# Performance work log

Hardware: AMD Instinct MI355X
Metric: run time of the kernel (lower is better)

## Reference

```python
import jax, jax.numpy as jnp
import numpy as np


def setup_inputs() -> dict:
    key = jax.random.key(0)
    k1, k2 = jax.random.split(key)
    B, C, H, W = 4, 256, 64, 64
    hw = 1024  # hs = ws = 32, rate = H/hs = 2
    ori_x = jax.random.normal(k1, (B, C, H, W), dtype=jnp.float32)
    scores = jax.random.uniform(k2, (B, hw, hw), dtype=jnp.float32)
    alpha = jnp.ones((1,), dtype=jnp.float32)
    return {"ori_x": ori_x, "scores": scores, "alpha": alpha}


def reference(ori_x, scores, alpha):
    # GroupConvAttention forward for H=W=64 (no bilinear resize branch taken,
    # matching the torch code's else-branch), rate even (no extra rep-pad).
    B, C, H, W = ori_x.shape
    hw = scores.shape[2]
    hs = int(np.sqrt(hw)); ws = hs
    rate = H // hs               # 2
    vk = 2 * rate                # vksize = 4
    pad = rate // 2              # vpadding = 1 (rate even)

    # extract_patches: ReplicationPad2d(pad) + unfold(kernel=vk, stride=rate)
    x_pad = jnp.pad(ori_x, ((0, 0), (0, 0), (pad, pad), (pad, pad)), mode="edge")
    # gather index grids: patch (m,n), intra-patch (u,v)
    ri = (jnp.arange(hs) * rate)[:, None] + jnp.arange(vk)[None, :]  # [hs, vk]
    ci = (jnp.arange(ws) * rate)[:, None] + jnp.arange(vk)[None, :]  # [ws, vk]
    R = ri[:, None, :, None]   # [hs,1,vk,1]
    Cc = ci[None, :, None, :]  # [1,ws,1,vk]
    value = x_pad[:, :, R, Cc]  # [B, C, hs, ws, vk, vk]

    # conv_transpose2d(scores_, value, stride=rate, padding=pad, groups=B)
    # == per query grid cell (Q,R): combined patch = sum_p scores[b,q,p]*value[b,p]
    s = scores.reshape(B, hs, ws, hs, ws)  # [b, Qy, Qx, my, mx]
    P = jnp.einsum("bQRmn,bcmnuv->bcQRuv", s, value)  # [B,C,hs,ws,vk,vk]

    # overlap-add patches at stride `rate` into padded canvas, then crop padding
    canvas = jnp.zeros((B, C, (hs - 1) * rate + vk, (ws - 1) * rate + vk), P.dtype)
    canvas = canvas.at[:, :, R, Cc].add(P)
    y = canvas[:, :, pad:pad + H, pad:pad + W] / 4.0

    return ori_x + y * alpha
```

## Files before the change

kernel.cpp:

```cpp
#include <hip/hip_runtime.h>
#include <hip/hip_bf16.h>
#include <hip/hip_fp16.h>

#define BB 4
#define CC 256
#define HH 64
#define WW 64
#define QRN 1024
#define KN  1024
#define NN  4096
#define KDIM 1120
#define MROWS 1024
#define TROWS 1089

typedef _Float16 f16x8 __attribute__((ext_vector_type(8)));
typedef float f32x4 __attribute__((ext_vector_type(4)));
typedef float f32x16 __attribute__((ext_vector_type(16)));

#define TP_ELEMS ((size_t)BB * TROWS * KDIM)
#define BP_ELEMS ((size_t)16 * CC * KDIM)


#define T_BLOCKS 1089
#define PER_B    1249
#define TB_NWG   (BB * PER_B)

__global__ __launch_bounds__(256)
void build_TB(const float* __restrict__ s, const float* __restrict__ x,
              _Float16* __restrict__ T, _Float16* __restrict__ Bp) {
    const int orig = blockIdx.x;
    const int xcd = orig & 7, pos = orig >> 3;
    const int q = TB_NWG / 8, r = TB_NWG % 8;
    const int wgid =
        (xcd < r ? xcd * (q + 1) : r * (q + 1) + (xcd - r) * q) + pos;

    const int b = wgid / PER_B;
    const int rem = wgid - b * PER_B;
    const int t = threadIdx.x;

    if (rem < T_BLOCKS) {
        const int qr = rem;
        const int Qa = (qr * 993) >> 15;
        const int Ra = qr - 33 * Qa;
        const bool q0 = (Qa < 32), q1 = (Qa >= 1);
        const bool r0 = (Ra < 32), r1 = (Ra >= 1);
        const float* sb = s + (size_t)b * QRN * KN;
        const float* rb00 = sb + ((size_t)((Qa)     * 32 + (Ra)))     * KN;
        const float* rb01 = sb + ((size_t)((Qa)     * 32 + (Ra - 1))) * KN;
        const float* rb10 = sb + ((size_t)((Qa - 1) * 32 + (Ra)))     * KN;
        const float* rb11 = sb + ((size_t)((Qa - 1) * 32 + (Ra - 1))) * KN;
        _Float16* trow = T + ((size_t)b * TROWS + qr) * KDIM;

        float v[5];
        #pragma unroll
        for (int j = 0; j < 5; ++j) {
            const int k = j * 256 + t;
            v[j] = 0.f;
            if (k < KDIM) {
                const int mp = (k * 993) >> 15;
                const int np = k - 33 * mp;
                const bool m0 = (mp < 32), m1 = (mp >= 1) && (mp < 33);
                const bool n0 = (np < 32), n1 = (np >= 1);
                const int col = (mp << 5) + np;
                if (q0 & r0 & m0 & n0) v[j] += rb00[col];
                if (q0 & r1 & m0 & n1) v[j] += rb01[col - 1];
                if (q1 & r0 & m1 & n0) v[j] += rb10[col - 32];
                if (q1 & r1 & m1 & n1) v[j] += rb11[col - 33];
            }
        }
        #pragma unroll
        for (int j = 0; j < 5; ++j) {
            const int k = j * 256 + t;
            if (k < KDIM) trow[k] = (_Float16)v[j];
        }
    } else {
        const int u = rem - T_BLOCKS;
        const int rest = u / 5;
        const int kc = u - rest * 5;
        const int cls = rest >> 3, cg = rest & 7;
        const int k = kc * 256 + t;
        if (k >= KDIM) return;
        const int ph = cls >> 1, pw = cls & 1;
        const int ua = 1 - ph, va = 1 - pw;
        const int bc = b * 4 + cls;

        const int mp = (k * 993) >> 15;
        const int np = k - 33 * mp;
        int rr = 2 * mp + ua - 1; rr = min(max(rr, 0), HH - 1);
        int cc2 = 2 * np + va - 1; cc2 = min(max(cc2, 0), WW - 1);
        const int off = rr * WW + cc2;

        const float* xb = x + ((size_t)b * CC + cg * 32) * HH * WW;
        _Float16* bpb = Bp + ((size_t)bc * CC + cg * 32) * KDIM + k;

        #pragma unroll 8
        for (int i = 0; i < 32; ++i) {
            bpb[(size_t)i * KDIM] = (_Float16)xb[(size_t)i * HH * WW + off];
        }
    }
}

#define A_SLOT 520
#define B_SLOT 1040
#define PF 4
#define NT 35
__global__ __launch_bounds__(256)
void gemm_f16(const _Float16* __restrict__ T,
              const _Float16* __restrict__ Bp,
              const float* __restrict__ orix,
              const float* __restrict__ alphap,
              float* __restrict__ out) {
    __shared__ __align__(16) char smem[32768];
    _Float16* AmB = (_Float16*)smem;
    _Float16* BnB = AmB + 2 * 4 * A_SLOT;
    float*    ex  = (float*)smem;

    const int lin = blockIdx.x + 4 * (blockIdx.y + 8 * blockIdx.z);
    const int wid = (lin & 7) * 64 + (lin >> 3);
    const int bc  = wid >> 5;
    const int byy = (wid >> 2) & 7;
    const int bxx = wid & 3;

    const int b = bc >> 2, cls = bc & 3;
    const int ph = cls >> 1, pw = cls & 1;
    const int c0  = bxx * 64;
    const int px0 = byy * 128;

    const int t = threadIdx.x;
    const int wv = t >> 6, l = t & 63;
    const int lr = l & 31;
    const int lh = l >> 5;
    const int wc = wv & 1;
    const int ks = wv >> 1;

    const _Float16* Ag = Bp + ((size_t)bc * CC + c0) * KDIM;
    const _Float16* Tg = T + (size_t)b * TROWS * KDIM;

    const int st_row  = t >> 2;
    const int st_slot = t & 3;
    const int pxa = px0 + st_row, pxb = px0 + st_row + 64;
    const int trow0 = ((pxa >> 5) + ph) * 33 + (pxa & 31) + pw;
    const int trow1 = ((pxb >> 5) + ph) * 33 + (pxb & 31) + pw;

    f32x16 acc[2][2];
    #pragma unroll
    for (int i = 0; i < 2; ++i)
        #pragma unroll
        for (int j = 0; j < 2; ++j)
            acc[i][j] = (f32x16)(0.f);

    f16x8 rga[PF], rgb0[PF], rgb1[PF];

    #pragma unroll
    for (int s2 = 0; s2 < PF; ++s2) {
        const size_t kb = s2 * 32 + st_slot * 8;
        rga[s2]  = *reinterpret_cast<const f16x8*>(Ag + (size_t)st_row * KDIM + kb);
        rgb0[s2] = *reinterpret_cast<const f16x8*>(Tg + (size_t)trow0 * KDIM + kb);
        rgb1[s2] = *reinterpret_cast<const f16x8*>(Tg + (size_t)trow1 * KDIM + kb);
    }
    *reinterpret_cast<f16x8*>(&AmB[st_slot * A_SLOT + st_row * 8]) = rga[0];
    *reinterpret_cast<f16x8*>(&BnB[st_slot * B_SLOT + st_row * 8]) = rgb0[0];
    *reinterpret_cast<f16x8*>(&BnB[st_slot * B_SLOT + (st_row + 64) * 8]) = rgb1[0];
    asm volatile("s_waitcnt lgkmcnt(0)" ::: "memory");
    __builtin_amdgcn_s_barrier();

    #pragma unroll
    for (int ts = 0; ts < NT; ++ts) {
        const int cur = ts & 1;
        if (ts + PF < NT) {
            const int sl = ts & 3;
            const size_t kb = (size_t)(ts + PF) * 32 + st_slot * 8;
            rga[sl]  = *reinterpret_cast<const f16x8*>(Ag + (size_t)st_row * KDIM + kb);
            rgb0[sl] = *reinterpret_cast<const f16x8*>(Tg + (size_t)trow0 * KDIM + kb);
            rgb1[sl] = *reinterpret_cast<const f16x8*>(Tg + (size_t)trow1 * KDIM + kb);
        }

        const int slot = ks * 2 + lh;
        f16x8 af[2], bf[2];
        #pragma unroll
        for (int mt = 0; mt < 2; ++mt)
            af[mt] = *reinterpret_cast<const f16x8*>(
                &AmB[cur * 4 * A_SLOT + slot * A_SLOT + (mt * 32 + lr) * 8]);
        #pragma unroll
        for (int nt2 = 0; nt2 < 2; ++nt2)
            bf[nt2] = *reinterpret_cast<const f16x8*>(
                &BnB[cur * 4 * B_SLOT + slot * B_SLOT +
                     (wc * 64 + nt2 * 32 + lr) * 8]);
        __builtin_amdgcn_s_setprio(1);
        #pragma unroll
        for (int mt = 0; mt < 2; ++mt)
            #pragma unroll
            for (int nt2 = 0; nt2 < 2; ++nt2)
                acc[mt][nt2] = __builtin_amdgcn_mfma_f32_32x32x16_f16(
                    af[mt], bf[nt2], acc[mt][nt2], 0, 0, 0);
        __builtin_amdgcn_s_setprio(0);

        if (ts + 1 < NT) {
            const int ns = (ts + 1) & 3, nb = cur ^ 1;
            *reinterpret_cast<f16x8*>(&AmB[nb * 4 * A_SLOT + st_slot * A_SLOT + st_row * 8]) = rga[ns];
            *reinterpret_cast<f16x8*>(&BnB[nb * 4 * B_SLOT + st_slot * B_SLOT + st_row * 8]) = rgb0[ns];
            *reinterpret_cast<f16x8*>(&BnB[nb * 4 * B_SLOT + st_slot * B_SLOT + (st_row + 64) * 8]) = rgb1[ns];
        }
        asm volatile("s_waitcnt lgkmcnt(0)" ::: "memory");
        __builtin_amdgcn_s_barrier();
    }

    if (ks == 1) {
        #pragma unroll
        for (int mt = 0; mt < 2; ++mt)
            #pragma unroll
            for (int nt2 = 0; nt2 < 2; ++nt2)
                #pragma unroll
                for (int r = 0; r < 16; ++r)
                    ex[((((mt * 2 + nt2) * 2 + wc) * 16) + r) * 64 + l] =
                        acc[mt][nt2][r];
    }
    asm volatile("s_waitcnt lgkmcnt(0)" ::: "memory");
    __builtin_amdgcn_s_barrier();

    if (ks == 0) {
        const float scale = 0.25f * alphap[0];
        #pragma unroll
        for (int mt = 0; mt < 2; ++mt) {
            #pragma unroll
            for (int nt2 = 0; nt2 < 2; ++nt2) {
                #pragma unroll
                for (int r = 0; r < 16; ++r) {
                    float vsum = acc[mt][nt2][r] +
                        ex[((((mt * 2 + nt2) * 2 + wc) * 16) + r) * 64 + l];
                    int c  = c0 + mt * 32 + (r & 3) + 8 * (r >> 2) + 4 * lh;
                    int px = px0 + wc * 64 + nt2 * 32 + lr;
                    int hh = px >> 5, ww2 = px & 31;
                    int h = 2 * hh + ph, wp = 2 * ww2 + pw;
                    size_t idx = (((size_t)b * CC + c) * HH + h) * WW + wp;
                    out[idx] = orix[idx] + scale * vsum;
                }
            }
        }
    }
}

#define TILE_M 64
#define TILE_N 64
#define TILE_K 16

__global__ void copy_kernel(const float* __restrict__ src,
                            float* __restrict__ dst, int n4) {
    int i = blockIdx.x * blockDim.x + threadIdx.x;
    if (i < n4)
        reinterpret_cast<float4*>(dst)[i] =
            reinterpret_cast<const float4*>(src)[i];
}

__global__ void transpose_kernel(const float* __restrict__ x,
                                 float* __restrict__ xT) {
    __shared__ float tile[32][33];
    int bh = blockIdx.z;
    int b = bh >> 6, h = bh & 63;
    int c0 = blockIdx.y * 32, w0 = blockIdx.x * 32;
    int tw = threadIdx.x & 31;
    int tc = threadIdx.x >> 5;
    #pragma unroll
    for (int i = 0; i < 4; ++i) {
        int c = tc + i * 8;
        tile[c][tw] = x[(((size_t)b * CC + c0 + c) * HH + h) * WW + w0 + tw];
    }
    __syncthreads();
    int tcw = threadIdx.x & 31;
    int twr = threadIdx.x >> 5;
    #pragma unroll
    for (int i = 0; i < 4; ++i) {
        int w = twr + i * 8;
        xT[(((size_t)b * HH + h) * WW + w0 + w) * CC + c0 + tcw] = tile[tcw][w];
    }
}

__global__ __launch_bounds__(256)
void pgemm_scatter(const float* __restrict__ scores,
                   const float* __restrict__ xT,
                   const float* __restrict__ x,
                   const float* __restrict__ alpha,
                   float* __restrict__ out,
                   int use_xt) {
    __shared__ float As[TILE_K][TILE_M];
    __shared__ float Bs[TILE_K][TILE_N];

    const int b      = blockIdx.z;
    const int tile_n = blockIdx.x;
    const int m0     = blockIdx.y * TILE_M;
    const int uv     = tile_n >> 2;
    const int u      = uv >> 2, v = uv & 3;
    const int c0     = (tile_n & 3) * 64;

    const int t  = threadIdx.x;
    const int tx = t & 15;
    const int ty = t >> 4;

    float acc[4][4] = {};
    const float* sb = scores + (size_t)b * QRN * KN;

    for (int k0 = 0; k0 < KN; k0 += TILE_K) {
        {
            int mr = t >> 2;
            int kc = (t & 3) * 4;
            float4 av = *reinterpret_cast<const float4*>(
                sb + (size_t)(m0 + mr) * KN + k0 + kc);
            As[kc + 0][mr] = av.x;
            As[kc + 1][mr] = av.y;
            As[kc + 2][mr] = av.z;
            As[kc + 3][mr] = av.w;
        }
        {
            int kr = t >> 4;
            int kg = k0 + kr;
            int m  = kg >> 5, n = kg & 31;
            int rr = 2 * m + u - 1; rr = min(max(rr, 0), HH - 1);
            int cc = 2 * n + v - 1; cc = min(max(cc, 0), WW - 1);
            int ccol = (t & 15) * 4;
            if (use_xt) {
                float4 bv = *reinterpret_cast<const float4*>(
                    xT + ((((size_t)b * HH + rr) * WW + cc) * CC) + c0 + ccol);
                Bs[kr][ccol + 0] = bv.x;
                Bs[kr][ccol + 1] = bv.y;
                Bs[kr][ccol + 2] = bv.z;
                Bs[kr][ccol + 3] = bv.w;
            } else {
                #pragma unroll
                for (int j = 0; j < 4; ++j) {
                    int c = c0 + ccol + j;
                    Bs[kr][ccol + j] =
                        x[(((size_t)b * CC + c) * HH + rr) * WW + cc];
                }
            }
        }
        __syncthreads();

        #pragma unroll
        for (int k = 0; k < TILE_K; ++k) {
            float a4[4], b4[4];
            *reinterpret_cast<float4*>(a4) =
                *reinterpret_cast<const float4*>(&As[k][ty * 4]);
            *reinterpret_cast<float4*>(b4) =
                *reinterpret_cast<const float4*>(&Bs[k][tx * 4]);
            #pragma unroll
            for (int i = 0; i < 4; ++i)
                #pragma unroll
                for (int j = 0; j < 4; ++j)
                    acc[i][j] += a4[i] * b4[j];
        }
        __syncthreads();
    }

    const float scale = alpha[0] * 0.25f;
    #pragma unroll
    for (int i = 0; i < 4; ++i) {
        int qr = m0 + ty * 4 + i;
        int Q = qr >> 5, R = qr & 31;
        int h = 2 * Q + u - 1;
        int w = 2 * R + v - 1;
        if (h < 0 || h >= HH || w < 0 || w >= WW) continue;
        #pragma unroll
        for (int j = 0; j < 4; ++j) {
            int c = c0 + tx * 4 + j;
            atomicAdd(&out[(((size_t)b * CC + c) * HH + h) * WW + w],
                      acc[i][j] * scale);
        }
    }
}

extern "C" void kernel_launch(void* const* d_in, const int* in_sizes, int n_in,
                              void* d_out, int out_size, void* d_ws,
                              size_t ws_size, hipStream_t stream) {
    const float* ori_x  = (const float*)d_in[0];
    const float* scores = (const float*)d_in[1];
    const float* alpha  = (const float*)d_in[2];
    float* out = (float*)d_out;

    const size_t need_fast = (TP_ELEMS + BP_ELEMS) * sizeof(_Float16);

    if (ws_size >= need_fast) {
        _Float16* T  = (_Float16*)d_ws;
        _Float16* Bp = T + TP_ELEMS;

        build_TB<<<dim3(TB_NWG), 256, 0, stream>>>(scores, ori_x, T, Bp);
        gemm_f16<<<dim3(4, 8, 16), 256, 0, stream>>>(T, Bp, ori_x, alpha, out);
    } else {
        float* xT = (float*)d_ws;
        const size_t xt_bytes = (size_t)BB * HH * WW * CC * sizeof(float);
        const int use_xt = (ws_size >= xt_bytes) ? 1 : 0;

        copy_kernel<<<(BB * CC * HH * WW / 4 + 255) / 256, 256, 0, stream>>>(
            ori_x, out, BB * CC * HH * WW / 4);
        if (use_xt)
            transpose_kernel<<<dim3(WW / 32, CC / 32, BB * HH), 256, 0,
                               stream>>>(ori_x, xT);
        pgemm_scatter<<<dim3(NN / TILE_N, QRN / TILE_M, BB), 256, 0, stream>>>(
            scores, xT, ori_x, alpha, out, use_xt);
    }
}
```

Measured before the change: 48.98 us.

## Double GEMM K-step per barrier and build two T rows per block

The f16 GEMM now consumes 64 K-elements per pipeline step instead of 32. Each thread stages more rows and slots, the register prefetch depth drops from 4 to 2, and LDS grows to about 49 KB. This roughly halves the number of barrier/LDS-store rounds and pads KDIM to 1152 so the steps divide evenly. The build kernel also handles two T rows per workgroup to cut launch overhead, at the cost of some extra padded work and higher register and LDS pressure.

```diff
diff --git a/kernel.cpp b/kernel.cpp
--- a/kernel.cpp
+++ b/kernel.cpp
@@ -8,9 +8,7 @@
 #define WW 64
 #define QRN 1024
 #define KN  1024
-#define NN  4096
-#define KDIM 1120
-#define MROWS 1024
+#define KDIM 1152
 #define TROWS 1089
 
 typedef _Float16 f16x8 __attribute__((ext_vector_type(8)));
@@ -21,8 +19,45 @@
 #define BP_ELEMS ((size_t)16 * CC * KDIM)
 
 
-#define T_BLOCKS 1089
-#define PER_B    1249
+__device__ __forceinline__
+void process_qr(const float* __restrict__ sb, _Float16* __restrict__ T,
+                int b, int qr, int t) {
+    const int Qa = (qr * 993) >> 15;
+    const int Ra = qr - 33 * Qa;
+    const bool q0 = (Qa < 32), q1 = (Qa >= 1);
+    const bool r0 = (Ra < 32), r1 = (Ra >= 1);
+    const float* rb00 = sb + ((size_t)((Qa)     * 32 + (Ra)))     * KN;
+    const float* rb01 = sb + ((size_t)((Qa)     * 32 + (Ra - 1))) * KN;
+    const float* rb10 = sb + ((size_t)((Qa - 1) * 32 + (Ra)))     * KN;
+    const float* rb11 = sb + ((size_t)((Qa - 1) * 32 + (Ra - 1))) * KN;
+    _Float16* trow = T + ((size_t)b * TROWS + qr) * KDIM;
+
+    float v[5];
+    #pragma unroll
+    for (int j = 0; j < 5; ++j) {
+        const int k = j * 256 + t;
+        v[j] = 0.f;
+        if (k < KDIM) {
+            const int mp = (k * 993) >> 15;
+            const int np = k - 33 * mp;
+            const bool m0 = (mp < 32), m1 = (mp >= 1) && (mp < 33);
+            const bool n0 = (np < 32), n1 = (np >= 1);
+            const int col = (mp << 5) + np;
+            if (q0 & r0 & m0 & n0) v[j] += rb00[col];
+            if (q0 & r1 & m0 & n1) v[j] += rb01[col - 1];
+            if (q1 & r0 & m1 & n0) v[j] += rb10[col - 32];
+            if (q1 & r1 & m1 & n1) v[j] += rb11[col - 33];
+        }
+    }
+    #pragma unroll
+    for (int j = 0; j < 5; ++j) {
+        const int k = j * 256 + t;
+        if (k < KDIM) trow[k] = (_Float16)v[j];
+    }
+}
+
+#define T_BLOCKS 545
+#define PER_B    705
 #define TB_NWG   (BB * PER_B)
 
 __global__ __launch_bounds__(256)
@@ -39,40 +74,10 @@
     const int t = threadIdx.x;
 
     if (rem < T_BLOCKS) {
-        const int qr = rem;
-        const int Qa = (qr * 993) >> 15;
-        const int Ra = qr - 33 * Qa;
-        const bool q0 = (Qa < 32), q1 = (Qa >= 1);
-        const bool r0 = (Ra < 32), r1 = (Ra >= 1);
         const float* sb = s + (size_t)b * QRN * KN;
-        const float* rb00 = sb + ((size_t)((Qa)     * 32 + (Ra)))     * KN;
-        const float* rb01 = sb + ((size_t)((Qa)     * 32 + (Ra - 1))) * KN;
-        const float* rb10 = sb + ((size_t)((Qa - 1) * 32 + (Ra)))     * KN;
-        const float* rb11 = sb + ((size_t)((Qa - 1) * 32 + (Ra - 1))) * KN;
-        _Float16* trow = T + ((size_t)b * TROWS + qr) * KDIM;
-
-        float v[5];
-        #pragma unroll
-        for (int j = 0; j < 5; ++j) {
-            const int k = j * 256 + t;
-            v[j] = 0.f;
-            if (k < KDIM) {
-                const int mp = (k * 993) >> 15;
-                const int np = k - 33 * mp;
-                const bool m0 = (mp < 32), m1 = (mp >= 1) && (mp < 33);
-                const bool n0 = (np < 32), n1 = (np >= 1);
-                const int col = (mp << 5) + np;
-                if (q0 & r0 & m0 & n0) v[j] += rb00[col];
-                if (q0 & r1 & m0 & n1) v[j] += rb01[col - 1];
-                if (q1 & r0 & m1 & n0) v[j] += rb10[col - 32];
-                if (q1 & r1 & m1 & n1) v[j] += rb11[col - 33];
-            }
-        }
-        #pragma unroll
-        for (int j = 0; j < 5; ++j) {
-            const int k = j * 256 + t;
-            if (k < KDIM) trow[k] = (_Float16)v[j];
-        }
+        const int qr0 = rem * 2;
+        process_qr(sb, T, b, qr0, t);
+        if (qr0 + 1 < TROWS) process_qr(sb, T, b, qr0 + 1, t);
     } else {
         const int u = rem - T_BLOCKS;
         const int rest = u / 5;
@@ -102,17 +107,18 @@
 
 #define A_SLOT 520
 #define B_SLOT 1040
-#define PF 4
-#define NT 35
+#define A_BUF  (8 * A_SLOT)
+#define B_BUF  (8 * B_SLOT)
+#define NSTEP  18
 __global__ __launch_bounds__(256)
 void gemm_f16(const _Float16* __restrict__ T,
               const _Float16* __restrict__ Bp,
               const float* __restrict__ orix,
               const float* __restrict__ alphap,
               float* __restrict__ out) {
-    __shared__ __align__(16) char smem[32768];
+    __shared__ __align__(16) char smem[49920];
     _Float16* AmB = (_Float16*)smem;
-    _Float16* BnB = AmB + 2 * 4 * A_SLOT;
+    _Float16* BnB = AmB + 2 * A_BUF;
     float*    ex  = (float*)smem;
 
     const int lin = blockIdx.x + 4 * (blockIdx.y + 8 * blockIdx.z);
@@ -136,11 +142,15 @@
     const _Float16* Ag = Bp + ((size_t)bc * CC + c0) * KDIM;
     const _Float16* Tg = T + (size_t)b * TROWS * KDIM;
 
-    const int st_row  = t >> 2;
-    const int st_slot = t & 3;
-    const int pxa = px0 + st_row, pxb = px0 + st_row + 64;
-    const int trow0 = ((pxa >> 5) + ph) * 33 + (pxa & 31) + pw;
-    const int trow1 = ((pxb >> 5) + ph) * 33 + (pxb & 31) + pw;
+    const int st_r    = t >> 3;
+    const int st_slot = t & 7;
+    const int kb0     = st_slot * 8;
+    int trowv[4];
+    #pragma unroll
+    for (int r2 = 0; r2 < 4; ++r2) {
+        const int px = px0 + r2 * 32 + st_r;
+        trowv[r2] = ((px >> 5) + ph) * 33 + (px & 31) + pw;
+    }
 
     f32x16 acc[2][2];
     #pragma unroll
@@ -149,57 +159,77 @@
         for (int j = 0; j < 2; ++j)
             acc[i][j] = (f32x16)(0.f);
 
-    f16x8 rga[PF], rgb0[PF], rgb1[PF];
-
-    #pragma unroll
-    for (int s2 = 0; s2 < PF; ++s2) {
-        const size_t kb = s2 * 32 + st_slot * 8;
-        rga[s2]  = *reinterpret_cast<const f16x8*>(Ag + (size_t)st_row * KDIM + kb);
-        rgb0[s2] = *reinterpret_cast<const f16x8*>(Tg + (size_t)trow0 * KDIM + kb);
-        rgb1[s2] = *reinterpret_cast<const f16x8*>(Tg + (size_t)trow1 * KDIM + kb);
-    }
-    *reinterpret_cast<f16x8*>(&AmB[st_slot * A_SLOT + st_row * 8]) = rga[0];
-    *reinterpret_cast<f16x8*>(&BnB[st_slot * B_SLOT + st_row * 8]) = rgb0[0];
-    *reinterpret_cast<f16x8*>(&BnB[st_slot * B_SLOT + (st_row + 64) * 8]) = rgb1[0];
+    f16x8 rga[2][2], rgb[2][4];
+
+    #pragma unroll
+    for (int s2 = 0; s2 < 2; ++s2) {
+        const size_t kb = (size_t)s2 * 64 + kb0;
+        rga[s2][0] = *reinterpret_cast<const f16x8*>(Ag + (size_t)st_r * KDIM + kb);
+        rga[s2][1] = *reinterpret_cast<const f16x8*>(Ag + (size_t)(st_r + 32) * KDIM + kb);
+        #pragma unroll
+        for (int r2 = 0; r2 < 4; ++r2)
+            rgb[s2][r2] = *reinterpret_cast<const f16x8*>(
+                Tg + (size_t)trowv[r2] * KDIM + kb);
+    }
+    *reinterpret_cast<f16x8*>(&AmB[st_slot * A_SLOT + st_r * 8]) = rga[0][0];
+    *reinterpret_cast<f16x8*>(&AmB[st_slot * A_SLOT + (st_r + 32) * 8]) = rga[0][1];
+    #pragma unroll
+    for (int r2 = 0; r2 < 4; ++r2)
+        *reinterpret_cast<f16x8*>(
+            &BnB[st_slot * B_SLOT + (r2 * 32 + st_r) * 8]) = rgb[0][r2];
     asm volatile("s_waitcnt lgkmcnt(0)" ::: "memory");
     __builtin_amdgcn_s_barrier();
 
     #pragma unroll
-    for (int ts = 0; ts < NT; ++ts) {
+    for (int ts = 0; ts < NSTEP; ++ts) {
         const int cur = ts & 1;
-        if (ts + PF < NT) {
-            const int sl = ts & 3;
-            const size_t kb = (size_t)(ts + PF) * 32 + st_slot * 8;
-            rga[sl]  = *reinterpret_cast<const f16x8*>(Ag + (size_t)st_row * KDIM + kb);
-            rgb0[sl] = *reinterpret_cast<const f16x8*>(Tg + (size_t)trow0 * KDIM + kb);
-            rgb1[sl] = *reinterpret_cast<const f16x8*>(Tg + (size_t)trow1 * KDIM + kb);
-        }
-
-        const int slot = ks * 2 + lh;
-        f16x8 af[2], bf[2];
-        #pragma unroll
-        for (int mt = 0; mt < 2; ++mt)
-            af[mt] = *reinterpret_cast<const f16x8*>(
-                &AmB[cur * 4 * A_SLOT + slot * A_SLOT + (mt * 32 + lr) * 8]);
-        #pragma unroll
-        for (int nt2 = 0; nt2 < 2; ++nt2)
-            bf[nt2] = *reinterpret_cast<const f16x8*>(
-                &BnB[cur * 4 * B_SLOT + slot * B_SLOT +
-                     (wc * 64 + nt2 * 32 + lr) * 8]);
+        if (ts + 2 < NSTEP) {
+            const int sl = ts & 1;
+            const size_t kb = (size_t)(ts + 2) * 64 + kb0;
+            rga[sl][0] = *reinterpret_cast<const f16x8*>(Ag + (size_t)st_r * KDIM + kb);
+            rga[sl][1] = *reinterpret_cast<const f16x8*>(Ag + (size_t)(st_r + 32) * KDIM + kb);
+            #pragma unroll
+            for (int r2 = 0; r2 < 4; ++r2)
+                rgb[sl][r2] = *reinterpret_cast<const f16x8*>(
+                    Tg + (size_t)trowv[r2] * KDIM + kb);
+        }
+
+        f16x8 af[2][2], bf[2][2];
+        #pragma unroll
+        for (int kk = 0; kk < 2; ++kk) {
+            const int slot = ks * 4 + kk * 2 + lh;
+            #pragma unroll
+            for (int mt = 0; mt < 2; ++mt)
+                af[mt][kk] = *reinterpret_cast<const f16x8*>(
+                    &AmB[cur * A_BUF + slot * A_SLOT + (mt * 32 + lr) * 8]);
+            #pragma unroll
+            for (int nt2 = 0; nt2 < 2; ++nt2)
+                bf[nt2][kk] = *reinterpret_cast<const f16x8*>(
+                    &BnB[cur * B_BUF + slot * B_SLOT +
+                         (wc * 64 + nt2 * 32 + lr) * 8]);
+        }
         __builtin_amdgcn_s_setprio(1);
         #pragma unroll
-        for (int mt = 0; mt < 2; ++mt)
-            #pragma unroll
-            for (int nt2 = 0; nt2 < 2; ++nt2)
-                acc[mt][nt2] = __builtin_amdgcn_mfma_f32_32x32x16_f16(
-                    af[mt], bf[nt2], acc[mt][nt2], 0, 0, 0);
+        for (int kk = 0; kk < 2; ++kk)
+            #pragma unroll
+            for (int mt = 0; mt < 2; ++mt)
+                #pragma unroll
+                for (int nt2 = 0; nt2 < 2; ++nt2)
+                    acc[mt][nt2] = __builtin_amdgcn_mfma_f32_32x32x16_f16(
+                        af[mt][kk], bf[nt2][kk], acc[mt][nt2], 0, 0, 0);
         __builtin_amdgcn_s_setprio(0);
 
-        if (ts + 1 < NT) {
-            const int ns = (ts + 1) & 3, nb = cur ^ 1;
-            *reinterpret_cast<f16x8*>(&AmB[nb * 4 * A_SLOT + st_slot * A_SLOT + st_row * 8]) = rga[ns];
-            *reinterpret_cast<f16x8*>(&BnB[nb * 4 * B_SLOT + st_slot * B_SLOT + st_row * 8]) = rgb0[ns];
-            *reinterpret_cast<f16x8*>(&BnB[nb * 4 * B_SLOT + st_slot * B_SLOT + (st_row + 64) * 8]) = rgb1[ns];
+        if (ts + 1 < NSTEP) {
+            const int ns = (ts + 1) & 1, nb = cur ^ 1;
+            *reinterpret_cast<f16x8*>(
+                &AmB[nb * A_BUF + st_slot * A_SLOT + st_r * 8]) = rga[ns][0];
+            *reinterpret_cast<f16x8*>(
+                &AmB[nb * A_BUF + st_slot * A_SLOT + (st_r + 32) * 8]) = rga[ns][1];
+            #pragma unroll
+            for (int r2 = 0; r2 < 4; ++r2)
+                *reinterpret_cast<f16x8*>(
+                    &BnB[nb * B_BUF + st_slot * B_SLOT +
+                         (r2 * 32 + st_r) * 8]) = rgb[ns][r2];
         }
         asm volatile("s_waitcnt lgkmcnt(0)" ::: "memory");
         __builtin_amdgcn_s_barrier();
@@ -211,9 +241,9 @@
             #pragma unroll
             for (int nt2 = 0; nt2 < 2; ++nt2)
                 #pragma unroll
-                for (int r = 0; r < 16; ++r)
-                    ex[((((mt * 2 + nt2) * 2 + wc) * 16) + r) * 64 + l] =
-                        acc[mt][nt2][r];
+                for (int r2 = 0; r2 < 16; ++r2)
+                    ex[((((mt * 2 + nt2) * 2 + wc) * 16) + r2) * 64 + l] =
+                        acc[mt][nt2][r2];
     }
     asm volatile("s_waitcnt lgkmcnt(0)" ::: "memory");
     __builtin_amdgcn_s_barrier();
@@ -225,10 +255,10 @@
             #pragma unroll
             for (int nt2 = 0; nt2 < 2; ++nt2) {
                 #pragma unroll
-                for (int r = 0; r < 16; ++r) {
-                    float vsum = acc[mt][nt2][r] +
-                        ex[((((mt * 2 + nt2) * 2 + wc) * 16) + r) * 64 + l];
-                    int c  = c0 + mt * 32 + (r & 3) + 8 * (r >> 2) + 4 * lh;
+                for (int r2 = 0; r2 < 16; ++r2) {
+                    float vsum = acc[mt][nt2][r2] +
+                        ex[((((mt * 2 + nt2) * 2 + wc) * 16) + r2) * 64 + l];
+                    int c  = c0 + mt * 32 + (r2 & 3) + 8 * (r2 >> 2) + 4 * lh;
                     int px = px0 + wc * 64 + nt2 * 32 + lr;
                     int hh = px >> 5, ww2 = px & 31;
                     int h = 2 * hh + ph, wp = 2 * ww2 + pw;
@@ -394,7 +424,7 @@
         if (use_xt)
             transpose_kernel<<<dim3(WW / 32, CC / 32, BB * HH), 256, 0,
                                stream>>>(ori_x, xT);
-        pgemm_scatter<<<dim3(NN / TILE_N, QRN / TILE_M, BB), 256, 0, stream>>>(
+        pgemm_scatter<<<dim3(16, 16, BB), 256, 0, stream>>>(
             scores, xT, ori_x, alpha, out, use_xt);
     }
 }
```

After: 49.00 us. About the same (+0.0%).
